# Optimization experiments

Hardware: AMD Instinct MI355X
Metric: run time of the kernel (lower is better)

The kernel has to match this reference:

```python
import jax, jax.numpy as jnp
import numpy as np

N, C, H, D, K = 16384, 256, 8, 64, 8
HID, OUT, NE = 512, 64, 64
COMMIT, RADIUS, RHID = 0.25, 10.0, 16


def setup_inputs() -> dict:
    key = jax.random.key(0)
    ks = jax.random.split(key, 20)
    def w(k, shape, fan_in):
        return jax.random.normal(k, shape, jnp.float32) / np.sqrt(fan_in).astype(np.float32)
    return {
        'x': jax.random.normal(ks[0], (N, C), jnp.float32),
        'coors': jax.random.normal(ks[1], (N, 3), jnp.float32) * 3.0,
        'nbr_idx': jax.random.randint(ks[2], (N, K), 0, N, jnp.int32),
        'Wq': w(ks[3], (C, H * D), C),
        'Wk': w(ks[4], (C, H * D), C),
        'Wv': w(ks[5], (C, H * D), C),
        'w_gate': w(ks[6], (C, H), C),
        'Wr1': w(ks[7], (1, RHID), 1),
        'br1': jnp.zeros((RHID,), jnp.float32),
        'Wr2': w(ks[8], (RHID, H), RHID),
        'br2': jnp.zeros((H,), jnp.float32),
        'Wo': w(ks[9], (H * D + H, C), H * D + H),
        'alpha1': jnp.float32(0.5) * jnp.ones((), jnp.float32),
        'gamma1': jnp.ones((C,), jnp.float32),
        'beta1': jnp.zeros((C,), jnp.float32),
        'Wlin': w(ks[10], (C, HID), C),
        'blin': jnp.zeros((HID,), jnp.float32),
        'alpha2': jnp.float32(0.5) * jnp.ones((), jnp.float32),
        'gamma2': jnp.ones((HID + 20,), jnp.float32),
        'beta2': jnp.zeros((HID + 20,), jnp.float32),
        'Wout': w(ks[11], (HID + 20, OUT), HID + 20),
        'bout': jnp.zeros((OUT,), jnp.float32),
        'codebook': jax.random.normal(ks[12], (NE, OUT), jnp.float32),
    }


def reference(x, coors, Wq, Wk, Wv, w_gate, Wr1, br1, Wr2, br2, Wo,
              alpha1, gamma1, beta1, Wlin, blin, alpha2, gamma2, beta2,
              Wout, bout, codebook, nbr_idx):
    # ---- SE(3)-equivariant sparse-neighbor attention (heads=8, dim_head=64, K=8) ----
    q = (x @ Wq).reshape(N, H, D)
    xn = x[nbr_idx]                                  # [N,K,C] neighbor gather
    k = (xn @ Wk).reshape(N, K, H, D)
    v = (xn @ Wv).reshape(N, K, H, D)
    rel = coors[nbr_idx] - coors[:, None, :]         # [N,K,3]
    dist = jnp.sqrt(jnp.sum(rel * rel, -1) + 1e-8)   # [N,K]
    unit = rel / dist[..., None]
    radial = jax.nn.gelu(dist[..., None] @ Wr1 + br1) @ Wr2 + br2   # [N,K,H]
    logits = jnp.einsum('nhd,nkhd->nkh', q, k) / np.float32(np.sqrt(D)) + radial
    logits = jnp.where((dist <= RADIUS)[..., None], logits, jnp.float32(-1e9))
    attn = jax.nn.softmax(logits, axis=1)            # over K neighbors
    out0 = jnp.einsum('nkh,nkhd->nhd', attn, v).reshape(N, H * D)   # degree-0
    gate = xn @ w_gate                               # [N,K,H]
    vec = jnp.einsum('nkh,nkx->nhx', attn * gate, unit)             # degree-1 [N,H,3]
    vecnorm = jnp.sqrt(jnp.sum(vec * vec, -1) + 1e-8)               # invariant [N,H]
    se3_out = x + jnp.concatenate([out0, vecnorm], -1) @ Wo         # residual
    # ---- lin: DynamicTanh -> Linear -> GELU ----
    h = jnp.tanh(alpha1 * se3_out) * gamma1 + beta1
    h = jax.nn.gelu(h @ Wlin + blin)
    # ---- out_dense: concat 20-dim aa feats, DynamicTanh -> Linear -> GELU -> Tanh ----
    h2 = jnp.concatenate([h, x[:, :20]], -1)
    h2 = jnp.tanh(alpha2 * h2) * gamma2 + beta2
    z = jnp.tanh(jax.nn.gelu(h2 @ Wout + bout))      # [N,OUT]
    # ---- VQ-EMA: nearest codebook entry, commitment loss, straight-through ----
    d2 = (jnp.sum(z * z, -1, keepdims=True)
          - 2.0 * z @ codebook.T
          + jnp.sum(codebook * codebook, -1))
    idx = jnp.argmin(d2, axis=-1)
    zq = codebook[idx]
    vq_loss = COMMIT * jnp.mean((z - jax.lax.stop_gradient(zq)) ** 2)
    z_quantized = z + jax.lax.stop_gradient(zq - z)
    return z_quantized, vq_loss
```

## Files before the change

### kernel.cpp

```cpp
#include <hip/hip_runtime.h>
#include <hip/hip_bf16.h>
#include <stdint.h>

#define NPTS 16384
#define CDIM 256
#define HEADS 8
#define KNBR 8
#define HIDD 512
#define OUTD 64
#define NEMB 64
#define RHIDD 16

typedef _Float16 half8 __attribute__((ext_vector_type(8)));
typedef float f32x4 __attribute__((ext_vector_type(4)));

__device__ __forceinline__ float gelu_tanh(float v) {
    float v3 = v * v * v;
    return 0.5f * v * (1.0f + tanhf(0.79788456080286535588f * (v + 0.044715f * v3)));
}

__device__ __forceinline__ void gload16(const void* g, void* l) {
    __builtin_amdgcn_global_load_lds((const __attribute__((address_space(1))) void*)g,
                                     (__attribute__((address_space(3))) void*)l, 16, 0, 0);
}

template <int EPI>
__launch_bounds__(256)
__global__ void gemm_split(const _Float16* __restrict__ A2, const _Float16* __restrict__ B2,
                           int Kpad, int KT,
                           void* __restrict__ Cout, int ldc,
                           const float* __restrict__ bias,
                           const float* __restrict__ res,
                           const float* __restrict__ alphap,
                           const float* __restrict__ gamma,
                           const float* __restrict__ beta,
                           const float* __restrict__ a2p,
                           const float* __restrict__ g2,
                           const float* __restrict__ b2,
                           void* __restrict__ aux) {
    __shared__ __align__(16) char lds[32768];

    const int tid = threadIdx.x;
    const int l = tid & 63, w = tid >> 6;
    const int g = l >> 4, r = l & 15;
    const int wr = w >> 1, wc = w & 1;
    const int m0 = blockIdx.y * 128;
    const int n0 = blockIdx.x * 128;
    const int ldA = 2 * Kpad;
    const int srow = l >> 3;
    const int sl = (l & 7) ^ srow;
    const int scol = (sl & 3) * 8 + ((sl >= 4) ? Kpad : 0);
    const int swz = (l & 7) << 4;
    const int aBase = (wr * 64 + r) * 128;
    const int bBase = 16384 + (wc * 64 + r) * 128;
    const int koh = (g << 4) ^ swz;
    const int kol = (64 | (g << 4)) ^ swz;

    f32x4 acc[4][4] = {};

    const _Float16* aS = A2 + (size_t)m0 * ldA + scol;
    const _Float16* bS = B2 + (size_t)n0 * ldA + scol;

    for (int t = 0; t < KT; ++t) {
        const int kk = t * 32;
        #pragma unroll
        for (int cc = 0; cc < 4; ++cc) {
            int ch = w * 4 + cc;
            int row = ch * 8 + srow;
            gload16(aS + (size_t)row * ldA + kk, lds + ch * 1024);
            gload16(bS + (size_t)row * ldA + kk, lds + 16384 + ch * 1024);
        }
        __syncthreads();
        half8 ah[4], bh[4], xf[4];
        #pragma unroll
        for (int i = 0; i < 4; ++i) ah[i] = *(const half8*)(lds + aBase + i * 2048 + koh);
        #pragma unroll
        for (int j = 0; j < 4; ++j) bh[j] = *(const half8*)(lds + bBase + j * 2048 + koh);
        #pragma unroll
        for (int i = 0; i < 4; ++i)
            #pragma unroll
            for (int j = 0; j < 4; ++j)
                acc[i][j] = __builtin_amdgcn_mfma_f32_16x16x32_f16(ah[i], bh[j], acc[i][j], 0, 0, 0);
        #pragma unroll
        for (int j = 0; j < 4; ++j) xf[j] = *(const half8*)(lds + bBase + j * 2048 + kol);
        #pragma unroll
        for (int i = 0; i < 4; ++i)
            #pragma unroll
            for (int j = 0; j < 4; ++j)
                acc[i][j] = __builtin_amdgcn_mfma_f32_16x16x32_f16(ah[i], xf[j], acc[i][j], 0, 0, 0);
        #pragma unroll
        for (int i = 0; i < 4; ++i) xf[i] = *(const half8*)(lds + aBase + i * 2048 + kol);
        #pragma unroll
        for (int i = 0; i < 4; ++i)
            #pragma unroll
            for (int j = 0; j < 4; ++j)
                acc[i][j] = __builtin_amdgcn_mfma_f32_16x16x32_f16(xf[i], bh[j], acc[i][j], 0, 0, 0);
        __syncthreads();
    }

    const float alp = (EPI == 1 || EPI == 2) ? alphap[0] : 0.f;
    #pragma unroll
    for (int i = 0; i < 4; ++i) {
        #pragma unroll
        for (int j = 0; j < 4; ++j) {
            const int gcol = n0 + wc * 64 + j * 16 + r;
            #pragma unroll
            for (int q = 0; q < 4; ++q) {
                const int row = m0 + wr * 64 + i * 16 + g * 4 + q;
                float v = acc[i][j][q];
                if (EPI == 0) {
                    if (gcol < 1536) {
                        ((float*)Cout)[(size_t)row * 1536 + gcol] = v;
                    } else if (gcol < 1544) {
                        ((float*)aux)[(size_t)row * 8 + (gcol - 1536)] = v;
                    }
                } else if (EPI == 1) {
                    v += res[(size_t)row * CDIM + gcol];
                    v = tanhf(alp * v) * gamma[gcol] + beta[gcol];
                    _Float16 hi = (_Float16)v;
                    _Float16 lo = (_Float16)(v - (float)hi);
                    _Float16* H = (_Float16*)Cout;
                    H[(size_t)row * 512 + gcol] = hi;
                    H[(size_t)row * 512 + 256 + gcol] = lo;
                    if (gcol < 64) {
                        int tc = 512 + gcol;
                        float tv = 0.f;
                        if (gcol < 20)
                            tv = tanhf(a2p[0] * res[(size_t)row * CDIM + gcol]) * g2[tc] + b2[tc];
                        _Float16 thi = (_Float16)tv;
                        _Float16 tlo = (_Float16)(tv - (float)thi);
                        _Float16* T = (_Float16*)aux;
                        T[(size_t)row * 1152 + tc] = thi;
                        T[(size_t)row * 1152 + 576 + tc] = tlo;
                    }
                } else if (EPI == 2) {
                    v = gelu_tanh(v + bias[gcol]);
                    v = tanhf(alp * v) * gamma[gcol] + beta[gcol];
                    _Float16 hi = (_Float16)v;
                    _Float16 lo = (_Float16)(v - (float)hi);
                    _Float16* H = (_Float16*)Cout;
                    H[(size_t)row * 1152 + gcol] = hi;
                    H[(size_t)row * 1152 + 576 + gcol] = lo;
                }
            }
        }
    }
}

__launch_bounds__(256)
__global__ void gemm_out_vq(const _Float16* __restrict__ A2, const _Float16* __restrict__ B2,
                            const float* __restrict__ bout, const float* __restrict__ cb,
                            float* __restrict__ outZ, float* __restrict__ partials) {
    __shared__ __align__(16) char lds[34816];
    __shared__ float psum[64];
    float* zL  = (float*)lds;
    float* cbL = (float*)(lds + 17408);

    const int tid = threadIdx.x;
    const int l = tid & 63, w = tid >> 6;
    const int g = l >> 4, r = l & 15;
    const int wr = w >> 1, wc = w & 1;
    const int m0 = blockIdx.x * 64;
    const int Kpad = 576;
    const int ldA = 1152;
    const int srow = l >> 3;
    const int sl = (l & 7) ^ srow;
    const int scol = (sl & 3) * 8 + ((sl >= 4) ? Kpad : 0);
    const int swz = (l & 7) << 4;
    const int aBase = (wr * 32 + r) * 128;
    const int bBase = 8192 + (wc * 32 + r) * 128;
    const int koh = (g << 4) ^ swz;
    const int kol = (64 | (g << 4)) ^ swz;

    f32x4 acc[2][2] = {};

    const _Float16* aS = A2 + (size_t)m0 * ldA + scol;
    const _Float16* bS = B2 + scol;

    for (int t = 0; t < 18; ++t) {
        const int kk = t * 32;
        #pragma unroll
        for (int cc = 0; cc < 2; ++cc) {
            int ch = w * 2 + cc;
            int row = ch * 8 + srow;
            gload16(aS + (size_t)row * ldA + kk, lds + ch * 1024);
            gload16(bS + (size_t)row * ldA + kk, lds + 8192 + ch * 1024);
        }
        __syncthreads();
        half8 ah[2], bh[2], xf[2];
        #pragma unroll
        for (int i = 0; i < 2; ++i) ah[i] = *(const half8*)(lds + aBase + i * 2048 + koh);
        #pragma unroll
        for (int j = 0; j < 2; ++j) bh[j] = *(const half8*)(lds + bBase + j * 2048 + koh);
        #pragma unroll
        for (int i = 0; i < 2; ++i)
            #pragma unroll
            for (int j = 0; j < 2; ++j)
                acc[i][j] = __builtin_amdgcn_mfma_f32_16x16x32_f16(ah[i], bh[j], acc[i][j], 0, 0, 0);
        #pragma unroll
        for (int j = 0; j < 2; ++j) xf[j] = *(const half8*)(lds + bBase + j * 2048 + kol);
        #pragma unroll
        for (int i = 0; i < 2; ++i)
            #pragma unroll
            for (int j = 0; j < 2; ++j)
                acc[i][j] = __builtin_amdgcn_mfma_f32_16x16x32_f16(ah[i], xf[j], acc[i][j], 0, 0, 0);
        #pragma unroll
        for (int i = 0; i < 2; ++i) xf[i] = *(const half8*)(lds + aBase + i * 2048 + kol);
        #pragma unroll
        for (int i = 0; i < 2; ++i)
            #pragma unroll
            for (int j = 0; j < 2; ++j)
                acc[i][j] = __builtin_amdgcn_mfma_f32_16x16x32_f16(xf[i], bh[j], acc[i][j], 0, 0, 0);
        __syncthreads();
    }

    #pragma unroll
    for (int i = 0; i < 2; ++i) {
        #pragma unroll
        for (int j = 0; j < 2; ++j) {
            int col = wc * 32 + j * 16 + r;
            #pragma unroll
            for (int q = 0; q < 4; ++q) {
                int rl = wr * 32 + i * 16 + g * 4 + q;
                zL[rl * 68 + col] = tanhf(gelu_tanh(acc[i][j][q] + bout[col]));
            }
        }
    }
    for (int i = tid; i < NEMB * OUTD / 4; i += 256) {
        float4 v = ((const float4*)cb)[i];
        int e = (i * 4) >> 6, c0 = (i * 4) & 63;
        cbL[e * 68 + c0 + 0] = v.x; cbL[e * 68 + c0 + 1] = v.y;
        cbL[e * 68 + c0 + 2] = v.z; cbL[e * 68 + c0 + 3] = v.w;
    }
    __syncthreads();
    if (tid < 64) {
        float cc = 0.f;
        #pragma unroll
        for (int d = 0; d < 64; ++d) { float cv = cbL[tid * 68 + d]; cc += cv * cv; }
        cbL[tid * 68 + 64] = cc;
    }
    __syncthreads();

    const int row = tid >> 2, part = tid & 3;
    float best = 1e30f;
    int bidx = 0;
    for (int e = part * 16; e < part * 16 + 16; ++e) {
        float dot = 0.f;
        #pragma unroll
        for (int d = 0; d < 64; ++d) dot += zL[row * 68 + d] * cbL[e * 68 + d];
        float sc = cbL[e * 68 + 64] - 2.f * dot;
        if (sc < best) { best = sc; bidx = e; }
    }
    #pragma unroll
    for (int m = 1; m <= 2; m <<= 1) {
        float ob = __shfl_xor(best, m, 64);
        int oi = __shfl_xor(bidx, m, 64);
        if (ob < best || (ob == best && oi < bidx)) { best = ob; bidx = oi; }
    }
    const int grow = m0 + row;
    float lsum = 0.f;
    #pragma unroll
    for (int u = 0; u < 16; ++u) {
        float cv = cbL[bidx * 68 + part * 16 + u];
        outZ[(size_t)grow * 64 + part * 16 + u] = cv;
        float df = zL[row * 68 + part * 16 + u] - cv;
        lsum += df * df;
    }
    lsum += __shfl_xor(lsum, 1, 64);
    lsum += __shfl_xor(lsum, 2, 64);
    if (part == 0) psum[row] = lsum;
    __syncthreads();
    if (tid < 64) {
        float v = psum[tid];
        #pragma unroll
        for (int m = 1; m < 64; m <<= 1) v += __shfl_xor(v, m, 64);
        if (tid == 0) partials[blockIdx.x] = v;
    }
}

__global__ void vq_reduce(const float* __restrict__ partials, float* __restrict__ out) {
    __shared__ float s[256];
    int tid = threadIdx.x;
    s[tid] = partials[tid];
    __syncthreads();
    for (int st = 128; st > 0; st >>= 1) {
        if (tid < st) s[tid] += s[tid + st];
        __syncthreads();
    }
    if (tid == 0) out[0] = 0.25f * s[0] / ((float)NPTS * (float)OUTD);
}

#define R0 (NPTS * CDIM)
#define S1 (1664 * 256)
#define S2 (256 * 576)
#define S3 (512 * 256)
#define S4 (64 * 576)
__global__ void prep(const float* __restrict__ x,
                     const float* __restrict__ Wq, const float* __restrict__ Wk,
                     const float* __restrict__ Wv, const float* __restrict__ w_gate,
                     const float* __restrict__ Wo, const float* __restrict__ Wlin,
                     const float* __restrict__ Wout,
                     _Float16* __restrict__ x2, _Float16* __restrict__ wqkv2,
                     _Float16* __restrict__ wo2, _Float16* __restrict__ wlin2,
                     _Float16* __restrict__ wout2) {
    for (int idx = blockIdx.x * 256 + threadIdx.x; idx < R0 + S1 + S2 + S3 + S4;
         idx += gridDim.x * 256) {
        float v; _Float16* dst; size_t o0, o1;
        if (idx < R0) {
            int n = idx >> 8, cc = idx & 255;
            v = x[idx];
            dst = x2; o0 = (size_t)n * 512 + cc; o1 = o0 + 256;
        } else if (idx < R0 + S1) {
            int t = idx - R0;
            int j = t >> 8, k = t & 255;
            if (j < 1536) {
                int jm = j & 511;
                const float* W = (j < 512) ? Wq : (j < 1024) ? Wk : Wv;
                v = W[(size_t)k * 512 + jm];
            } else if (j < 1544) {
                v = w_gate[(size_t)k * 8 + (j - 1536)];
            } else {
                v = 0.f;
            }
            dst = wqkv2; o0 = (size_t)j * 512 + k; o1 = o0 + 256;
        } else if (idx < R0 + S1 + S2) {
            int t = idx - R0 - S1;
            int j = t / 576, k = t - j * 576;
            v = (k < 520) ? Wo[(size_t)k * 256 + j] : 0.f;
            dst = wo2; o0 = (size_t)j * 1152 + k; o1 = o0 + 576;
        } else if (idx < R0 + S1 + S2 + S3) {
            int t = idx - R0 - S1 - S2;
            int j = t >> 8, k = t & 255;
            v = Wlin[(size_t)k * 512 + j];
            dst = wlin2; o0 = (size_t)j * 512 + k; o1 = o0 + 256;
        } else {
            int t = idx - R0 - S1 - S2 - S3;
            int j = t / 576, k = t - j * 576;
            v = (k < 532) ? Wout[(size_t)k * 64 + j] : 0.f;
            dst = wout2; o0 = (size_t)j * 1152 + k; o1 = o0 + 576;
        }
        _Float16 hi = (_Float16)v, lo = (_Float16)(v - (float)hi);
        dst[o0] = hi; dst[o1] = lo;
    }
}

__launch_bounds__(256)
__global__ void attn_kernel(const float* __restrict__ QKV, const float* __restrict__ G,
                            const float* __restrict__ coors, const int* __restrict__ nbr,
                            const float* __restrict__ Wr1, const float* __restrict__ br1,
                            const float* __restrict__ Wr2, const float* __restrict__ br2,
                            _Float16* __restrict__ att2) {
    __shared__ float unitL[4][8][3];
    __shared__ float distL[4][8];
    __shared__ float radH[4][8][16];

    const int tid = threadIdx.x;
    const int w = tid >> 6;
    const int lane = tid & 63;
    const int n = blockIdx.x * 4 + w;
    const int h = lane >> 3;
    const int c = lane & 7;

    int jreg[KNBR];
    #pragma unroll
    for (int k = 0; k < KNBR; ++k) jreg[k] = nbr[(size_t)n * KNBR + k];

    if (lane < KNBR) {
        int jj = jreg[lane];
        float rx = coors[(size_t)jj * 3 + 0] - coors[(size_t)n * 3 + 0];
        float ry = coors[(size_t)jj * 3 + 1] - coors[(size_t)n * 3 + 1];
        float rz = coors[(size_t)jj * 3 + 2] - coors[(size_t)n * 3 + 2];
        float d = sqrtf(rx * rx + ry * ry + rz * rz + 1e-8f);
        float inv = 1.0f / d;
        distL[w][lane] = d;
        unitL[w][lane][0] = rx * inv;
        unitL[w][lane][1] = ry * inv;
        unitL[w][lane][2] = rz * inv;
    }

    const float4* qp = (const float4*)(QKV + (size_t)n * 1536 + lane * 8);
    float4 q0 = qp[0], q1 = qp[1];
    float p[KNBR];
    #pragma unroll
    for (int k = 0; k < KNBR; ++k) {
        const float4* kp = (const float4*)(QKV + (size_t)jreg[k] * 1536 + 512 + lane * 8);
        float4 k0 = kp[0], k1 = kp[1];
        p[k] = q0.x * k0.x + q0.y * k0.y + q0.z * k0.z + q0.w * k0.w
             + q1.x * k1.x + q1.y * k1.y + q1.z * k1.z + q1.w * k1.w;
    }
    #pragma unroll
    for (int m = 1; m <= 4; m <<= 1) {
        #pragma unroll
        for (int k = 0; k < KNBR; ++k) p[k] += __shfl_xor(p[k], m, 64);
    }
    __syncthreads();

    #pragma unroll
    for (int rr = 0; rr < 2; ++rr) {
        int idx = lane + rr * 64;
        int k = idx >> 4, i = idx & 15;
        float hv = distL[w][k] * Wr1[i] + br1[i];
        radH[w][k][i] = gelu_tanh(hv);
    }
    __syncthreads();

    float lg[KNBR];
    float b2v = br2[h];
    #pragma unroll
    for (int k = 0; k < KNBR; ++k) {
        float rad = b2v;
        #pragma unroll
        for (int i = 0; i < RHIDD; ++i) rad += radH[w][k][i] * Wr2[i * HEADS + h];
        lg[k] = p[k] * 0.125f + rad;
        if (!(distL[w][k] <= 10.0f)) lg[k] = -1e9f;
    }
    float mx = lg[0];
    #pragma unroll
    for (int k = 1; k < KNBR; ++k) mx = fmaxf(mx, lg[k]);
    float a[KNBR];
    float s = 0.f;
    #pragma unroll
    for (int k = 0; k < KNBR; ++k) { a[k] = expf(lg[k] - mx); s += a[k]; }
    float is = 1.0f / s;
    #pragma unroll
    for (int k = 0; k < KNBR; ++k) a[k] *= is;

    float vx = 0.f, vy = 0.f, vz = 0.f;
    #pragma unroll
    for (int k = 0; k < KNBR; ++k) {
        float gg = G[(size_t)jreg[k] * HEADS + h];
        float ag = a[k] * gg;
        vx += ag * unitL[w][k][0];
        vy += ag * unitL[w][k][1];
        vz += ag * unitL[w][k][2];
    }
    float vn = sqrtf(vx * vx + vy * vy + vz * vz + 1e-8f);

    float4 o0 = {0.f, 0.f, 0.f, 0.f}, o1 = {0.f, 0.f, 0.f, 0.f};
    #pragma unroll
    for (int k = 0; k < KNBR; ++k) {
        const float4* vp = (const float4*)(QKV + (size_t)jreg[k] * 1536 + 1024 + lane * 8);
        float4 v0 = vp[0], v1 = vp[1];
        float ak = a[k];
        o0.x += ak * v0.x; o0.y += ak * v0.y; o0.z += ak * v0.z; o0.w += ak * v0.w;
        o1.x += ak * v1.x; o1.y += ak * v1.y; o1.z += ak * v1.z; o1.w += ak * v1.w;
    }

    float ov[8] = {o0.x, o0.y, o0.z, o0.w, o1.x, o1.y, o1.z, o1.w};
    half8 hi8, lo8;
    #pragma unroll
    for (int t = 0; t < 8; ++t) {
        _Float16 hi = (_Float16)ov[t];
        hi8[t] = hi;
        lo8[t] = (_Float16)(ov[t] - (float)hi);
    }
    *(half8*)(att2 + (size_t)n * 1152 + lane * 8) = hi8;
    *(half8*)(att2 + (size_t)n * 1152 + 576 + lane * 8) = lo8;
    if (c == 0) {
        _Float16 hi = (_Float16)vn, lo = (_Float16)(vn - (float)hi);
        att2[(size_t)n * 1152 + 512 + h] = hi;
        att2[(size_t)n * 1152 + 576 + 512 + h] = lo;
    }
    if (lane < 56) {
        att2[(size_t)n * 1152 + 520 + lane] = (_Float16)0.f;
        att2[(size_t)n * 1152 + 1096 + lane] = (_Float16)0.f;
    }
}

extern "C" void kernel_launch(void* const* d_in, const int* in_sizes, int n_in,
                              void* d_out, int out_size, void* d_ws, size_t ws_size,
                              hipStream_t stream) {
    const float* x      = (const float*)d_in[0];
    const float* coors  = (const float*)d_in[1];
    const int*   nbr    = (const int*)  d_in[2];
    const float* Wq     = (const float*)d_in[3];
    const float* Wk     = (const float*)d_in[4];
    const float* Wv     = (const float*)d_in[5];
    const float* w_gate = (const float*)d_in[6];
    const float* Wr1    = (const float*)d_in[7];
    const float* br1    = (const float*)d_in[8];
    const float* Wr2    = (const float*)d_in[9];
    const float* br2    = (const float*)d_in[10];
    const float* Wo     = (const float*)d_in[11];
    const float* alpha1 = (const float*)d_in[12];
    const float* gamma1 = (const float*)d_in[13];
    const float* beta1  = (const float*)d_in[14];
    const float* Wlin   = (const float*)d_in[15];
    const float* blin   = (const float*)d_in[16];
    const float* alpha2 = (const float*)d_in[17];
    const float* gamma2 = (const float*)d_in[18];
    const float* beta2  = (const float*)d_in[19];
    const float* Wout   = (const float*)d_in[20];
    const float* bout   = (const float*)d_in[21];
    const float* cb     = (const float*)d_in[22];

    char* wsb = (char*)d_ws;
    float*    QKV   = (float*)   (wsb + 0);
    _Float16* att2  = (_Float16*)(wsb + 100663296);
    _Float16* x2    = (_Float16*)(wsb + 138412032);
    _Float16* wqkv2 = (_Float16*)(wsb + 155189248);
    _Float16* wo2   = (_Float16*)(wsb + 156893184);
    _Float16* wlin2 = (_Float16*)(wsb + 157483008);
    _Float16* wout2 = (_Float16*)(wsb + 158007296);
    float*    G     = (float*)   (wsb + 158154752);
    float*    part  = (float*)   (wsb + 158679040);
    _Float16* h1s   = (_Float16*)(wsb + 0);
    _Float16* h2s   = (_Float16*)(wsb + 20299776);

    float* outZ    = (float*)d_out;
    float* outLoss = outZ + (size_t)NPTS * OUTD;

    dim3 blk(256);

    prep<<<dim3(2048), blk, 0, stream>>>(x, Wq, Wk, Wv, w_gate, Wo, Wlin, Wout,
                                         x2, wqkv2, wo2, wlin2, wout2);
    gemm_split<0><<<dim3(13, 128), blk, 0, stream>>>(x2, wqkv2, 256, 8, QKV, 1536,
        nullptr, nullptr, nullptr, nullptr, nullptr, nullptr, nullptr, nullptr, G);
    attn_kernel<<<dim3(NPTS / 4), blk, 0, stream>>>(QKV, G, coors, nbr, Wr1, br1, Wr2, br2, att2);
    gemm_split<1><<<dim3(2, 128), blk, 0, stream>>>(att2, wo2, 576, 18, h1s, 0,
        nullptr, x, alpha1, gamma1, beta1, alpha2, gamma2, beta2, h2s);
    gemm_split<2><<<dim3(4, 128), blk, 0, stream>>>(h1s, wlin2, 256, 8, h2s, 0,
        blin, nullptr, alpha2, gamma2, beta2, nullptr, nullptr, nullptr, nullptr);
    gemm_out_vq<<<dim3(256), blk, 0, stream>>>(h2s, wout2, bout, cb, outZ, part);
    vq_reduce<<<dim3(1), blk, 0, stream>>>(part, outLoss);
}
```

Measured before the change: 397.8 us.

## Double-buffer LDS tiles in later GEMMs and fold VQ loss reduction into atomics

```diff
diff --git a/kernel.cpp b/kernel.cpp
--- a/kernel.cpp
+++ b/kernel.cpp
@@ -24,7 +24,7 @@
                                      (__attribute__((address_space(3))) void*)l, 16, 0, 0);
 }
 
-template <int EPI>
+template <int EPI, int DBUF>
 __launch_bounds__(256)
 __global__ void gemm_split(const _Float16* __restrict__ A2, const _Float16* __restrict__ B2,
                            int Kpad, int KT,
@@ -38,7 +38,8 @@
                            const float* __restrict__ g2,
                            const float* __restrict__ b2,
                            void* __restrict__ aux) {
-    __shared__ __align__(16) char lds[32768];
+    constexpr int LBYTES = DBUF ? 65536 : 32768;
+    __shared__ __align__(16) char lds[LBYTES];
 
     const int tid = threadIdx.x;
     const int l = tid & 63, w = tid >> 6;
@@ -61,41 +62,66 @@
     const _Float16* aS = A2 + (size_t)m0 * ldA + scol;
     const _Float16* bS = B2 + (size_t)n0 * ldA + scol;
 
-    for (int t = 0; t < KT; ++t) {
+    auto stage = [&](int buf, int t) {
         const int kk = t * 32;
+        char* d0 = lds + buf * 32768;
         #pragma unroll
         for (int cc = 0; cc < 4; ++cc) {
             int ch = w * 4 + cc;
             int row = ch * 8 + srow;
-            gload16(aS + (size_t)row * ldA + kk, lds + ch * 1024);
-            gload16(bS + (size_t)row * ldA + kk, lds + 16384 + ch * 1024);
-        }
-        __syncthreads();
+            gload16(aS + (size_t)row * ldA + kk, d0 + ch * 1024);
+            gload16(bS + (size_t)row * ldA + kk, d0 + 16384 + ch * 1024);
+        }
+    };
+    auto passes = [&](const char* Lb) {
         half8 ah[4], bh[4], xf[4];
         #pragma unroll
-        for (int i = 0; i < 4; ++i) ah[i] = *(const half8*)(lds + aBase + i * 2048 + koh);
-        #pragma unroll
-        for (int j = 0; j < 4; ++j) bh[j] = *(const half8*)(lds + bBase + j * 2048 + koh);
+        for (int i = 0; i < 4; ++i) ah[i] = *(const half8*)(Lb + aBase + i * 2048 + koh);
+        #pragma unroll
+        for (int j = 0; j < 4; ++j) bh[j] = *(const half8*)(Lb + bBase + j * 2048 + koh);
         #pragma unroll
         for (int i = 0; i < 4; ++i)
             #pragma unroll
             for (int j = 0; j < 4; ++j)
                 acc[i][j] = __builtin_amdgcn_mfma_f32_16x16x32_f16(ah[i], bh[j], acc[i][j], 0, 0, 0);
         #pragma unroll
-        for (int j = 0; j < 4; ++j) xf[j] = *(const half8*)(lds + bBase + j * 2048 + kol);
+        for (int j = 0; j < 4; ++j) xf[j] = *(const half8*)(Lb + bBase + j * 2048 + kol);
         #pragma unroll
         for (int i = 0; i < 4; ++i)
             #pragma unroll
             for (int j = 0; j < 4; ++j)
                 acc[i][j] = __builtin_amdgcn_mfma_f32_16x16x32_f16(ah[i], xf[j], acc[i][j], 0, 0, 0);
         #pragma unroll
-        for (int i = 0; i < 4; ++i) xf[i] = *(const half8*)(lds + aBase + i * 2048 + kol);
+        for (int i = 0; i < 4; ++i) xf[i] = *(const half8*)(Lb + aBase + i * 2048 + kol);
         #pragma unroll
         for (int i = 0; i < 4; ++i)
             #pragma unroll
             for (int j = 0; j < 4; ++j)
                 acc[i][j] = __builtin_amdgcn_mfma_f32_16x16x32_f16(xf[i], bh[j], acc[i][j], 0, 0, 0);
-        __syncthreads();
+    };
+
+    if (DBUF) {
+        stage(0, 0);
+        for (int t = 0; t < KT; ++t) {
+            const int cur = t & 1;
+            if (t + 1 < KT) {
+                stage(cur ^ 1, t + 1);
+                asm volatile("s_waitcnt vmcnt(8)" ::: "memory");
+            } else {
+                asm volatile("s_waitcnt vmcnt(0)" ::: "memory");
+            }
+            __builtin_amdgcn_s_barrier();
+            __builtin_amdgcn_sched_barrier(0);
+            passes(lds + cur * 32768);
+            __builtin_amdgcn_s_barrier();
+        }
+    } else {
+        for (int t = 0; t < KT; ++t) {
+            stage(0, t);
+            __syncthreads();
+            passes(lds);
+            __syncthreads();
+        }
     }
 
     const float alp = (EPI == 1 || EPI == 2) ? alphap[0] : 0.f;
@@ -150,7 +176,7 @@
 __launch_bounds__(256)
 __global__ void gemm_out_vq(const _Float16* __restrict__ A2, const _Float16* __restrict__ B2,
                             const float* __restrict__ bout, const float* __restrict__ cb,
-                            float* __restrict__ outZ, float* __restrict__ partials) {
+                            float* __restrict__ outZ, float* __restrict__ outLoss) {
     __shared__ __align__(16) char lds[34816];
     __shared__ float psum[64];
     float* zL  = (float*)lds;
@@ -177,41 +203,55 @@
     const _Float16* aS = A2 + (size_t)m0 * ldA + scol;
     const _Float16* bS = B2 + scol;
 
-    for (int t = 0; t < 18; ++t) {
+    auto stage = [&](int buf, int t) {
         const int kk = t * 32;
+        char* d0 = lds + buf * 16384;
         #pragma unroll
         for (int cc = 0; cc < 2; ++cc) {
             int ch = w * 2 + cc;
             int row = ch * 8 + srow;
-            gload16(aS + (size_t)row * ldA + kk, lds + ch * 1024);
-            gload16(bS + (size_t)row * ldA + kk, lds + 8192 + ch * 1024);
-        }
-        __syncthreads();
+            gload16(aS + (size_t)row * ldA + kk, d0 + ch * 1024);
+            gload16(bS + (size_t)row * ldA + kk, d0 + 8192 + ch * 1024);
+        }
+    };
+
+    stage(0, 0);
+    for (int t = 0; t < 18; ++t) {
+        const int cur = t & 1;
+        if (t + 1 < 18) {
+            stage(cur ^ 1, t + 1);
+            asm volatile("s_waitcnt vmcnt(4)" ::: "memory");
+        } else {
+            asm volatile("s_waitcnt vmcnt(0)" ::: "memory");
+        }
+        __builtin_amdgcn_s_barrier();
+        __builtin_amdgcn_sched_barrier(0);
+        const char* Lb = lds + cur * 16384;
         half8 ah[2], bh[2], xf[2];
         #pragma unroll
-        for (int i = 0; i < 2; ++i) ah[i] = *(const half8*)(lds + aBase + i * 2048 + koh);
-        #pragma unroll
-        for (int j = 0; j < 2; ++j) bh[j] = *(const half8*)(lds + bBase + j * 2048 + koh);
+        for (int i = 0; i < 2; ++i) ah[i] = *(const half8*)(Lb + aBase + i * 2048 + koh);
+        #pragma unroll
+        for (int j = 0; j < 2; ++j) bh[j] = *(const half8*)(Lb + bBase + j * 2048 + koh);
         #pragma unroll
         for (int i = 0; i < 2; ++i)
             #pragma unroll
             for (int j = 0; j < 2; ++j)
                 acc[i][j] = __builtin_amdgcn_mfma_f32_16x16x32_f16(ah[i], bh[j], acc[i][j], 0, 0, 0);
         #pragma unroll
-        for (int j = 0; j < 2; ++j) xf[j] = *(const half8*)(lds + bBase + j * 2048 + kol);
+        for (int j = 0; j < 2; ++j) xf[j] = *(const half8*)(Lb + bBase + j * 2048 + kol);
         #pragma unroll
         for (int i = 0; i < 2; ++i)
             #pragma unroll
             for (int j = 0; j < 2; ++j)
                 acc[i][j] = __builtin_amdgcn_mfma_f32_16x16x32_f16(ah[i], xf[j], acc[i][j], 0, 0, 0);
         #pragma unroll
-        for (int i = 0; i < 2; ++i) xf[i] = *(const half8*)(lds + aBase + i * 2048 + kol);
+        for (int i = 0; i < 2; ++i) xf[i] = *(const half8*)(Lb + aBase + i * 2048 + kol);
         #pragma unroll
         for (int i = 0; i < 2; ++i)
             #pragma unroll
             for (int j = 0; j < 2; ++j)
                 acc[i][j] = __builtin_amdgcn_mfma_f32_16x16x32_f16(xf[i], bh[j], acc[i][j], 0, 0, 0);
-        __syncthreads();
+        __builtin_amdgcn_s_barrier();
     }
 
     #pragma unroll
@@ -274,20 +314,9 @@
         float v = psum[tid];
         #pragma unroll
         for (int m = 1; m < 64; m <<= 1) v += __shfl_xor(v, m, 64);
-        if (tid == 0) partials[blockIdx.x] = v;
-    }
-}
-
-__global__ void vq_reduce(const float* __restrict__ partials, float* __restrict__ out) {
-    __shared__ float s[256];
-    int tid = threadIdx.x;
-    s[tid] = partials[tid];
-    __syncthreads();
-    for (int st = 128; st > 0; st >>= 1) {
-        if (tid < st) s[tid] += s[tid + st];
-        __syncthreads();
-    }
-    if (tid == 0) out[0] = 0.25f * s[0] / ((float)NPTS * (float)OUTD);
+        if (tid == 0)
+            atomicAdd(outLoss, v * (0.25f / ((float)NPTS * (float)OUTD)));
+    }
 }
 
 #define R0 (NPTS * CDIM)
@@ -302,7 +331,8 @@
                      const float* __restrict__ Wout,
                      _Float16* __restrict__ x2, _Float16* __restrict__ wqkv2,
                      _Float16* __restrict__ wo2, _Float16* __restrict__ wlin2,
-                     _Float16* __restrict__ wout2) {
+                     _Float16* __restrict__ wout2, float* __restrict__ outLoss) {
+    if (blockIdx.x == 0 && threadIdx.x == 0) *outLoss = 0.f;
     for (int idx = blockIdx.x * 256 + threadIdx.x; idx < R0 + S1 + S2 + S3 + S4;
          idx += gridDim.x * 256) {
         float v; _Float16* dst; size_t o0, o1;
@@ -503,7 +533,6 @@
     _Float16* wlin2 = (_Float16*)(wsb + 157483008);
     _Float16* wout2 = (_Float16*)(wsb + 158007296);
     float*    G     = (float*)   (wsb + 158154752);
-    float*    part  = (float*)   (wsb + 158679040);
     _Float16* h1s   = (_Float16*)(wsb + 0);
     _Float16* h2s   = (_Float16*)(wsb + 20299776);
 
@@ -513,14 +542,13 @@
     dim3 blk(256);
 
     prep<<<dim3(2048), blk, 0, stream>>>(x, Wq, Wk, Wv, w_gate, Wo, Wlin, Wout,
-                                         x2, wqkv2, wo2, wlin2, wout2);
-    gemm_split<0><<<dim3(13, 128), blk, 0, stream>>>(x2, wqkv2, 256, 8, QKV, 1536,
+                                         x2, wqkv2, wo2, wlin2, wout2, outLoss);
+    gemm_split<0, 0><<<dim3(13, 128), blk, 0, stream>>>(x2, wqkv2, 256, 8, QKV, 1536,
         nullptr, nullptr, nullptr, nullptr, nullptr, nullptr, nullptr, nullptr, G);
     attn_kernel<<<dim3(NPTS / 4), blk, 0, stream>>>(QKV, G, coors, nbr, Wr1, br1, Wr2, br2, att2);
-    gemm_split<1><<<dim3(2, 128), blk, 0, stream>>>(att2, wo2, 576, 18, h1s, 0,
+    gemm_split<1, 1><<<dim3(2, 128), blk, 0, stream>>>(att2, wo2, 576, 18, h1s, 0,
         nullptr, x, alpha1, gamma1, beta1, alpha2, gamma2, beta2, h2s);
-    gemm_split<2><<<dim3(4, 128), blk, 0, stream>>>(h1s, wlin2, 256, 8, h2s, 0,
+    gemm_split<2, 1><<<dim3(4, 128), blk, 0, stream>>>(h1s, wlin2, 256, 8, h2s, 0,
         blin, nullptr, alpha2, gamma2, beta2, nullptr, nullptr, nullptr, nullptr);
-    gemm_out_vq<<<dim3(256), blk, 0, stream>>>(h2s, wout2, bout, cb, outZ, part);
-    vq_reduce<<<dim3(1), blk, 0, stream>>>(part, outLoss);
-}
+    gemm_out_vq<<<dim3(256), blk, 0, stream>>>(h2s, wout2, bout, cb, outZ, outLoss);
+}
```

Measured after the change: 379.9 us. -4.5%, faster.

## Fuse Wo, Wlin, Wout GEMMs and VQ into one per-row-tile tail kernel

Applied to the files above, without the earlier changes.

```diff
diff --git a/kernel.cpp b/kernel.cpp
--- a/kernel.cpp
+++ b/kernel.cpp
@@ -24,20 +24,9 @@
                                      (__attribute__((address_space(3))) void*)l, 16, 0, 0);
 }
 
-template <int EPI>
 __launch_bounds__(256)
-__global__ void gemm_split(const _Float16* __restrict__ A2, const _Float16* __restrict__ B2,
-                           int Kpad, int KT,
-                           void* __restrict__ Cout, int ldc,
-                           const float* __restrict__ bias,
-                           const float* __restrict__ res,
-                           const float* __restrict__ alphap,
-                           const float* __restrict__ gamma,
-                           const float* __restrict__ beta,
-                           const float* __restrict__ a2p,
-                           const float* __restrict__ g2,
-                           const float* __restrict__ b2,
-                           void* __restrict__ aux) {
+__global__ void gemm_qkv(const _Float16* __restrict__ A2, const _Float16* __restrict__ B2,
+                         float* __restrict__ QKV, float* __restrict__ G) {
     __shared__ __align__(16) char lds[32768];
 
     const int tid = threadIdx.x;
@@ -46,10 +35,10 @@
     const int wr = w >> 1, wc = w & 1;
     const int m0 = blockIdx.y * 128;
     const int n0 = blockIdx.x * 128;
-    const int ldA = 2 * Kpad;
+    const int ldA = 512;
     const int srow = l >> 3;
     const int sl = (l & 7) ^ srow;
-    const int scol = (sl & 3) * 8 + ((sl >= 4) ? Kpad : 0);
+    const int scol = (sl & 3) * 8 + ((sl >= 4) ? 256 : 0);
     const int swz = (l & 7) << 4;
     const int aBase = (wr * 64 + r) * 128;
     const int bBase = 16384 + (wc * 64 + r) * 128;
@@ -61,7 +50,7 @@
     const _Float16* aS = A2 + (size_t)m0 * ldA + scol;
     const _Float16* bS = B2 + (size_t)n0 * ldA + scol;
 
-    for (int t = 0; t < KT; ++t) {
+    for (int t = 0; t < 8; ++t) {
         const int kk = t * 32;
         #pragma unroll
         for (int cc = 0; cc < 4; ++cc) {
@@ -98,7 +87,6 @@
         __syncthreads();
     }
 
-    const float alp = (EPI == 1 || EPI == 2) ? alphap[0] : 0.f;
     #pragma unroll
     for (int i = 0; i < 4; ++i) {
         #pragma unroll
@@ -108,39 +96,10 @@
             for (int q = 0; q < 4; ++q) {
                 const int row = m0 + wr * 64 + i * 16 + g * 4 + q;
                 float v = acc[i][j][q];
-                if (EPI == 0) {
-                    if (gcol < 1536) {
-                        ((float*)Cout)[(size_t)row * 1536 + gcol] = v;
-                    } else if (gcol < 1544) {
-                        ((float*)aux)[(size_t)row * 8 + (gcol - 1536)] = v;
-                    }
-                } else if (EPI == 1) {
-                    v += res[(size_t)row * CDIM + gcol];
-                    v = tanhf(alp * v) * gamma[gcol] + beta[gcol];
-                    _Float16 hi = (_Float16)v;
-                    _Float16 lo = (_Float16)(v - (float)hi);
-                    _Float16* H = (_Float16*)Cout;
-                    H[(size_t)row * 512 + gcol] = hi;
-                    H[(size_t)row * 512 + 256 + gcol] = lo;
-                    if (gcol < 64) {
-                        int tc = 512 + gcol;
-                        float tv = 0.f;
-                        if (gcol < 20)
-                            tv = tanhf(a2p[0] * res[(size_t)row * CDIM + gcol]) * g2[tc] + b2[tc];
-                        _Float16 thi = (_Float16)tv;
-                        _Float16 tlo = (_Float16)(tv - (float)thi);
-                        _Float16* T = (_Float16*)aux;
-                        T[(size_t)row * 1152 + tc] = thi;
-                        T[(size_t)row * 1152 + 576 + tc] = tlo;
-                    }
-                } else if (EPI == 2) {
-                    v = gelu_tanh(v + bias[gcol]);
-                    v = tanhf(alp * v) * gamma[gcol] + beta[gcol];
-                    _Float16 hi = (_Float16)v;
-                    _Float16 lo = (_Float16)(v - (float)hi);
-                    _Float16* H = (_Float16*)Cout;
-                    H[(size_t)row * 1152 + gcol] = hi;
-                    H[(size_t)row * 1152 + 576 + gcol] = lo;
+                if (gcol < 1536) {
+                    QKV[(size_t)row * 1536 + gcol] = v;
+                } else if (gcol < 1544) {
+                    G[(size_t)row * 8 + (gcol - 1536)] = v;
                 }
             }
         }
@@ -148,82 +107,233 @@
 }
 
 __launch_bounds__(256)
-__global__ void gemm_out_vq(const _Float16* __restrict__ A2, const _Float16* __restrict__ B2,
-                            const float* __restrict__ bout, const float* __restrict__ cb,
-                            float* __restrict__ outZ, float* __restrict__ partials) {
-    __shared__ __align__(16) char lds[34816];
-    __shared__ float psum[64];
-    float* zL  = (float*)lds;
-    float* cbL = (float*)(lds + 17408);
+__global__ void mega_tail(const _Float16* __restrict__ att2,
+                          const _Float16* __restrict__ wo2,
+                          const _Float16* __restrict__ wlin2,
+                          const _Float16* __restrict__ wout2,
+                          const float* __restrict__ x,
+                          const float* __restrict__ alpha1p, const float* __restrict__ gamma1,
+                          const float* __restrict__ beta1, const float* __restrict__ blin,
+                          const float* __restrict__ alpha2p, const float* __restrict__ gamma2,
+                          const float* __restrict__ beta2, const float* __restrict__ bout,
+                          const float* __restrict__ cb,
+                          float* __restrict__ outZ, float* __restrict__ outLoss) {
+    __shared__ __align__(16) char lds[122880];
+    char* const h1L = lds;
+    char* const R1  = lds + 32768;
+    char* const R2  = lds + 106496;
 
     const int tid = threadIdx.x;
     const int l = tid & 63, w = tid >> 6;
     const int g = l >> 4, r = l & 15;
     const int wr = w >> 1, wc = w & 1;
-    const int m0 = blockIdx.x * 64;
-    const int Kpad = 576;
-    const int ldA = 1152;
+    const int m0 = blockIdx.x * 32;
     const int srow = l >> 3;
     const int sl = (l & 7) ^ srow;
-    const int scol = (sl & 3) * 8 + ((sl >= 4) ? Kpad : 0);
-    const int swz = (l & 7) << 4;
-    const int aBase = (wr * 32 + r) * 128;
-    const int bBase = 8192 + (wc * 32 + r) * 128;
+    const int scol576 = (sl & 3) * 8 + ((sl >= 4) ? 576 : 0);
+    const int scol256 = (sl & 3) * 8 + ((sl >= 4) ? 256 : 0);
+    const int swz = (r & 7) << 4;
     const int koh = (g << 4) ^ swz;
     const int kol = (64 | (g << 4)) ^ swz;
-
-    f32x4 acc[2][2] = {};
-
-    const _Float16* aS = A2 + (size_t)m0 * ldA + scol;
-    const _Float16* bS = B2 + scol;
-
-    for (int t = 0; t < 18; ++t) {
-        const int kk = t * 32;
-        #pragma unroll
-        for (int cc = 0; cc < 2; ++cc) {
-            int ch = w * 2 + cc;
-            int row = ch * 8 + srow;
-            gload16(aS + (size_t)row * ldA + kk, lds + ch * 1024);
-            gload16(bS + (size_t)row * ldA + kk, lds + 8192 + ch * 1024);
-        }
-        __syncthreads();
-        half8 ah[2], bh[2], xf[2];
-        #pragma unroll
-        for (int i = 0; i < 2; ++i) ah[i] = *(const half8*)(lds + aBase + i * 2048 + koh);
-        #pragma unroll
-        for (int j = 0; j < 2; ++j) bh[j] = *(const half8*)(lds + bBase + j * 2048 + koh);
-        #pragma unroll
-        for (int i = 0; i < 2; ++i)
-            #pragma unroll
-            for (int j = 0; j < 2; ++j)
-                acc[i][j] = __builtin_amdgcn_mfma_f32_16x16x32_f16(ah[i], bh[j], acc[i][j], 0, 0, 0);
-        #pragma unroll
-        for (int j = 0; j < 2; ++j) xf[j] = *(const half8*)(lds + bBase + j * 2048 + kol);
-        #pragma unroll
-        for (int i = 0; i < 2; ++i)
-            #pragma unroll
-            for (int j = 0; j < 2; ++j)
-                acc[i][j] = __builtin_amdgcn_mfma_f32_16x16x32_f16(ah[i], xf[j], acc[i][j], 0, 0, 0);
-        #pragma unroll
-        for (int i = 0; i < 2; ++i) xf[i] = *(const half8*)(lds + aBase + i * 2048 + kol);
-        #pragma unroll
-        for (int i = 0; i < 2; ++i)
-            #pragma unroll
-            for (int j = 0; j < 2; ++j)
-                acc[i][j] = __builtin_amdgcn_mfma_f32_16x16x32_f16(xf[i], bh[j], acc[i][j], 0, 0, 0);
-        __syncthreads();
-    }
-
-    #pragma unroll
-    for (int i = 0; i < 2; ++i) {
-        #pragma unroll
-        for (int j = 0; j < 2; ++j) {
-            int col = wc * 32 + j * 16 + r;
-            #pragma unroll
-            for (int q = 0; q < 4; ++q) {
-                int rl = wr * 32 + i * 16 + g * 4 + q;
-                zL[rl * 68 + col] = tanhf(gelu_tanh(acc[i][j][q] + bout[col]));
-            }
+    const float a1 = alpha1p[0], a2 = alpha2p[0];
+
+    f32x4 acc0[8] = {};
+    {
+        auto stage0 = [&](int buf, int kt) {
+            char* d = R1 + buf * 36864;
+            const int kk = kt * 32;
+            gload16(att2 + (size_t)(m0 + w * 8 + srow) * 1152 + kk + scol576, d + w * 1024);
+            #pragma unroll
+            for (int i = 0; i < 8; ++i) {
+                int ch = w * 8 + i;
+                gload16(wo2 + (size_t)(ch * 8 + srow) * 1152 + kk + scol576,
+                        d + 4096 + ch * 1024);
+            }
+        };
+        stage0(0, 0);
+        for (int kt = 0; kt < 18; ++kt) {
+            const int cur = kt & 1;
+            if (kt + 1 < 18) {
+                stage0(cur ^ 1, kt + 1);
+                asm volatile("s_waitcnt vmcnt(9)" ::: "memory");
+            } else {
+                asm volatile("s_waitcnt vmcnt(0)" ::: "memory");
+            }
+            __builtin_amdgcn_s_barrier();
+            __builtin_amdgcn_sched_barrier(0);
+            const char* d = R1 + cur * 36864;
+            const int arow = wr * 16 + r;
+            const char* aAddr = d + (arow >> 3) * 1024 + (arow & 7) * 128;
+            half8 a_h = *(const half8*)(aAddr + koh);
+            half8 a_l = *(const half8*)(aAddr + kol);
+            #pragma unroll
+            for (int jf = 0; jf < 8; ++jf) {
+                const int brow = wc * 128 + jf * 16 + r;
+                const char* bAddr = d + 4096 + (brow >> 3) * 1024 + (brow & 7) * 128;
+                half8 b_h = *(const half8*)(bAddr + koh);
+                half8 b_l = *(const half8*)(bAddr + kol);
+                acc0[jf] = __builtin_amdgcn_mfma_f32_16x16x32_f16(a_h, b_h, acc0[jf], 0, 0, 0);
+                acc0[jf] = __builtin_amdgcn_mfma_f32_16x16x32_f16(a_h, b_l, acc0[jf], 0, 0, 0);
+                acc0[jf] = __builtin_amdgcn_mfma_f32_16x16x32_f16(a_l, b_h, acc0[jf], 0, 0, 0);
+            }
+            __builtin_amdgcn_s_barrier();
+        }
+    }
+    #pragma unroll
+    for (int jf = 0; jf < 8; ++jf) {
+        #pragma unroll
+        for (int q = 0; q < 4; ++q) {
+            const int row = wr * 16 + g * 4 + q;
+            const int col = wc * 128 + jf * 16 + r;
+            float v = acc0[jf][q] + x[(size_t)(m0 + row) * CDIM + col];
+            v = tanhf(a1 * v) * gamma1[col] + beta1[col];
+            _Float16 hi = (_Float16)v;
+            _Float16 lo = (_Float16)(v - (float)hi);
+            const int ktw = col >> 5, kloc = col & 31;
+            const int Lhi = ((kloc >> 3) << 4) | ((kloc & 7) << 1);
+            const int sw = (row & 7) << 4;
+            char* base = h1L + ktw * 4096 + (row >> 3) * 1024 + (row & 7) * 128;
+            *(_Float16*)(base + (Lhi ^ sw)) = hi;
+            *(_Float16*)(base + ((Lhi | 64) ^ sw)) = lo;
+        }
+    }
+    {
+        const int rw = tid >> 3, c8 = tid & 7;
+        #pragma unroll
+        for (int u = 0; u < 8; ++u) {
+            const int col = c8 * 8 + u;
+            float v = 0.f;
+            if (col < 20)
+                v = tanhf(a2 * x[(size_t)(m0 + rw) * CDIM + col]) * gamma2[512 + col] + beta2[512 + col];
+            _Float16 hi = (_Float16)v;
+            _Float16 lo = (_Float16)(v - (float)hi);
+            const int ktw = 16 + (col >> 5), kloc = col & 31;
+            const int Lhi = ((kloc >> 3) << 4) | ((kloc & 7) << 1);
+            const int sw = (rw & 7) << 4;
+            char* base = R1 + ktw * 4096 + (rw >> 3) * 1024 + (rw & 7) * 128;
+            *(_Float16*)(base + (Lhi ^ sw)) = hi;
+            *(_Float16*)(base + ((Lhi | 64) ^ sw)) = lo;
+        }
+    }
+    __syncthreads();
+
+    {
+        f32x4 accB[2] = {};
+        accB[0] = (f32x4){0.f, 0.f, 0.f, 0.f};
+        accB[1] = (f32x4){0.f, 0.f, 0.f, 0.f};
+        auto stageB = [&](int it) {
+            const int c2 = it >> 3, kt2 = it & 7;
+            char* d = R2 + (it & 1) * 8192;
+            #pragma unroll
+            for (int i = 0; i < 2; ++i) {
+                int ch = w * 2 + i;
+                gload16(wlin2 + (size_t)(c2 * 64 + ch * 8 + srow) * 512 + kt2 * 32 + scol256,
+                        d + ch * 1024);
+            }
+        };
+        stageB(0);
+        for (int it = 0; it < 64; ++it) {
+            if (it + 1 < 64) {
+                stageB(it + 1);
+                asm volatile("s_waitcnt vmcnt(2)" ::: "memory");
+            } else {
+                asm volatile("s_waitcnt vmcnt(0)" ::: "memory");
+            }
+            __builtin_amdgcn_s_barrier();
+            __builtin_amdgcn_sched_barrier(0);
+            const int kt = it & 7;
+            const char* d = R2 + (it & 1) * 8192;
+            const int arow = wr * 16 + r;
+            const char* aAddr = h1L + kt * 4096 + (arow >> 3) * 1024 + (arow & 7) * 128;
+            half8 a_h = *(const half8*)(aAddr + koh);
+            half8 a_l = *(const half8*)(aAddr + kol);
+            #pragma unroll
+            for (int jf = 0; jf < 2; ++jf) {
+                const int brow = wc * 32 + jf * 16 + r;
+                const char* bAddr = d + (brow >> 3) * 1024 + (brow & 7) * 128;
+                half8 b_h = *(const half8*)(bAddr + koh);
+                half8 b_l = *(const half8*)(bAddr + kol);
+                accB[jf] = __builtin_amdgcn_mfma_f32_16x16x32_f16(a_h, b_h, accB[jf], 0, 0, 0);
+                accB[jf] = __builtin_amdgcn_mfma_f32_16x16x32_f16(a_h, b_l, accB[jf], 0, 0, 0);
+                accB[jf] = __builtin_amdgcn_mfma_f32_16x16x32_f16(a_l, b_h, accB[jf], 0, 0, 0);
+            }
+            if ((it & 7) == 7) {
+                const int c2 = it >> 3;
+                #pragma unroll
+                for (int jf = 0; jf < 2; ++jf) {
+                    #pragma unroll
+                    for (int q = 0; q < 4; ++q) {
+                        const int row = wr * 16 + g * 4 + q;
+                        const int colg = c2 * 64 + wc * 32 + jf * 16 + r;
+                        float v = gelu_tanh(accB[jf][q] + blin[colg]);
+                        v = tanhf(a2 * v) * gamma2[colg] + beta2[colg];
+                        _Float16 hi = (_Float16)v;
+                        _Float16 lo = (_Float16)(v - (float)hi);
+                        const int ktw = colg >> 5, kloc = colg & 31;
+                        const int Lhi = ((kloc >> 3) << 4) | ((kloc & 7) << 1);
+                        const int sw = (row & 7) << 4;
+                        char* base = R1 + ktw * 4096 + (row >> 3) * 1024 + (row & 7) * 128;
+                        *(_Float16*)(base + (Lhi ^ sw)) = hi;
+                        *(_Float16*)(base + ((Lhi | 64) ^ sw)) = lo;
+                    }
+                    accB[jf] = (f32x4){0.f, 0.f, 0.f, 0.f};
+                }
+            }
+            __builtin_amdgcn_s_barrier();
+        }
+    }
+    __syncthreads();
+
+    f32x4 accC[2] = {};
+    {
+        auto stageC = [&](int kt) {
+            char* d = R2 + (kt & 1) * 8192;
+            #pragma unroll
+            for (int i = 0; i < 2; ++i) {
+                int ch = w * 2 + i;
+                gload16(wout2 + (size_t)(ch * 8 + srow) * 1152 + kt * 32 + scol576,
+                        d + ch * 1024);
+            }
+        };
+        stageC(0);
+        for (int kt = 0; kt < 18; ++kt) {
+            if (kt + 1 < 18) {
+                stageC(kt + 1);
+                asm volatile("s_waitcnt vmcnt(2)" ::: "memory");
+            } else {
+                asm volatile("s_waitcnt vmcnt(0)" ::: "memory");
+            }
+            __builtin_amdgcn_s_barrier();
+            __builtin_amdgcn_sched_barrier(0);
+            const char* d = R2 + (kt & 1) * 8192;
+            const int arow = wr * 16 + r;
+            const char* aAddr = R1 + kt * 4096 + (arow >> 3) * 1024 + (arow & 7) * 128;
+            half8 a_h = *(const half8*)(aAddr + koh);
+            half8 a_l = *(const half8*)(aAddr + kol);
+            #pragma unroll
+            for (int jf = 0; jf < 2; ++jf) {
+                const int brow = wc * 32 + jf * 16 + r;
+                const char* bAddr = d + (brow >> 3) * 1024 + (brow & 7) * 128;
+                half8 b_h = *(const half8*)(bAddr + koh);
+                half8 b_l = *(const half8*)(bAddr + kol);
+                accC[jf] = __builtin_amdgcn_mfma_f32_16x16x32_f16(a_h, b_h, accC[jf], 0, 0, 0);
+                accC[jf] = __builtin_amdgcn_mfma_f32_16x16x32_f16(a_h, b_l, accC[jf], 0, 0, 0);
+                accC[jf] = __builtin_amdgcn_mfma_f32_16x16x32_f16(a_l, b_h, accC[jf], 0, 0, 0);
+            }
+            __builtin_amdgcn_s_barrier();
+        }
+    }
+
+    float* zL   = (float*)lds;
+    float* cbL  = (float*)(lds + 8704);
+    float* psum = (float*)(lds + 26112);
+    #pragma unroll
+    for (int jf = 0; jf < 2; ++jf) {
+        #pragma unroll
+        for (int q = 0; q < 4; ++q) {
+            const int row = wr * 16 + g * 4 + q;
+            const int col = wc * 32 + jf * 16 + r;
+            zL[row * 68 + col] = tanhf(gelu_tanh(accC[jf][q] + bout[col]));
         }
     }
     for (int i = tid; i < NEMB * OUTD / 4; i += 256) {
@@ -241,10 +351,10 @@
     }
     __syncthreads();
 
-    const int row = tid >> 2, part = tid & 3;
+    const int row = tid >> 3, part = tid & 7;
     float best = 1e30f;
     int bidx = 0;
-    for (int e = part * 16; e < part * 16 + 16; ++e) {
+    for (int e = part * 8; e < part * 8 + 8; ++e) {
         float dot = 0.f;
         #pragma unroll
         for (int d = 0; d < 64; ++d) dot += zL[row * 68 + d] * cbL[e * 68 + d];
@@ -252,45 +362,35 @@
         if (sc < best) { best = sc; bidx = e; }
     }
     #pragma unroll
-    for (int m = 1; m <= 2; m <<= 1) {
+    for (int m = 1; m <= 4; m <<= 1) {
         float ob = __shfl_xor(best, m, 64);
         int oi = __shfl_xor(bidx, m, 64);
         if (ob < best || (ob == best && oi < bidx)) { best = ob; bidx = oi; }
     }
-    const int grow = m0 + row;
     float lsum = 0.f;
     #pragma unroll
-    for (int u = 0; u < 16; ++u) {
-        float cv = cbL[bidx * 68 + part * 16 + u];
-        outZ[(size_t)grow * 64 + part * 16 + u] = cv;
-        float df = zL[row * 68 + part * 16 + u] - cv;
+    for (int u = 0; u < 8; ++u) {
+        const int col = part * 8 + u;
+        float cv = cbL[bidx * 68 + col];
+        outZ[(size_t)(m0 + row) * 64 + col] = cv;
+        float df = zL[row * 68 + col] - cv;
         lsum += df * df;
     }
     lsum += __shfl_xor(lsum, 1, 64);
     lsum += __shfl_xor(lsum, 2, 64);
+    lsum += __shfl_xor(lsum, 4, 64);
     if (part == 0) psum[row] = lsum;
     __syncthreads();
-    if (tid < 64) {
+    if (tid < 32) {
         float v = psum[tid];
         #pragma unroll
-        for (int m = 1; m < 64; m <<= 1) v += __shfl_xor(v, m, 64);
-        if (tid == 0) partials[blockIdx.x] = v;
+        for (int m = 1; m < 32; m <<= 1) v += __shfl_xor(v, m, 64);
+        if (tid == 0)
+            atomicAdd(outLoss, v * (0.25f / ((float)NPTS * (float)OUTD)));
     }
 }
 
-__global__ void vq_reduce(const float* __restrict__ partials, float* __restrict__ out) {
-    __shared__ float s[256];
-    int tid = threadIdx.x;
-    s[tid] = partials[tid];
-    __syncthreads();
-    for (int st = 128; st > 0; st >>= 1) {
-        if (tid < st) s[tid] += s[tid + st];
-        __syncthreads();
-    }
-    if (tid == 0) out[0] = 0.25f * s[0] / ((float)NPTS * (float)OUTD);
-}
-
-#define R0 (NPTS * CDIM)
+#define R0SZ (NPTS * CDIM)
 #define S1 (1664 * 256)
 #define S2 (256 * 576)
 #define S3 (512 * 256)
@@ -302,16 +402,17 @@
                      const float* __restrict__ Wout,
                      _Float16* __restrict__ x2, _Float16* __restrict__ wqkv2,
                      _Float16* __restrict__ wo2, _Float16* __restrict__ wlin2,
-                     _Float16* __restrict__ wout2) {
-    for (int idx = blockIdx.x * 256 + threadIdx.x; idx < R0 + S1 + S2 + S3 + S4;
+                     _Float16* __restrict__ wout2, float* __restrict__ outLoss) {
+    if (blockIdx.x == 0 && threadIdx.x == 0) *outLoss = 0.f;
+    for (int idx = blockIdx.x * 256 + threadIdx.x; idx < R0SZ + S1 + S2 + S3 + S4;
          idx += gridDim.x * 256) {
         float v; _Float16* dst; size_t o0, o1;
-        if (idx < R0) {
+        if (idx < R0SZ) {
             int n = idx >> 8, cc = idx & 255;
             v = x[idx];
             dst = x2; o0 = (size_t)n * 512 + cc; o1 = o0 + 256;
-        } else if (idx < R0 + S1) {
-            int t = idx - R0;
+        } else if (idx < R0SZ + S1) {
+            int t = idx - R0SZ;
             int j = t >> 8, k = t & 255;
             if (j < 1536) {
                 int jm = j & 511;
@@ -323,18 +424,18 @@
                 v = 0.f;
             }
             dst = wqkv2; o0 = (size_t)j * 512 + k; o1 = o0 + 256;
-        } else if (idx < R0 + S1 + S2) {
-            int t = idx - R0 - S1;
+        } else if (idx < R0SZ + S1 + S2) {
+            int t = idx - R0SZ - S1;
             int j = t / 576, k = t - j * 576;
             v = (k < 520) ? Wo[(size_t)k * 256 + j] : 0.f;
             dst = wo2; o0 = (size_t)j * 1152 + k; o1 = o0 + 576;
-        } else if (idx < R0 + S1 + S2 + S3) {
-            int t = idx - R0 - S1 - S2;
+        } else if (idx < R0SZ + S1 + S2 + S3) {
+            int t = idx - R0SZ - S1 - S2;
             int j = t >> 8, k = t & 255;
             v = Wlin[(size_t)k * 512 + j];
             dst = wlin2; o0 = (size_t)j * 512 + k; o1 = o0 + 256;
         } else {
-            int t = idx - R0 - S1 - S2 - S3;
+            int t = idx - R0SZ - S1 - S2 - S3;
             int j = t / 576, k = t - j * 576;
             v = (k < 532) ? Wout[(size_t)k * 64 + j] : 0.f;
             dst = wout2; o0 = (size_t)j * 1152 + k; o1 = o0 + 576;
@@ -503,9 +604,6 @@
     _Float16* wlin2 = (_Float16*)(wsb + 157483008);
     _Float16* wout2 = (_Float16*)(wsb + 158007296);
     float*    G     = (float*)   (wsb + 158154752);
-    float*    part  = (float*)   (wsb + 158679040);
-    _Float16* h1s   = (_Float16*)(wsb + 0);
-    _Float16* h2s   = (_Float16*)(wsb + 20299776);
 
     float* outZ    = (float*)d_out;
     float* outLoss = outZ + (size_t)NPTS * OUTD;
@@ -513,14 +611,9 @@
     dim3 blk(256);
 
     prep<<<dim3(2048), blk, 0, stream>>>(x, Wq, Wk, Wv, w_gate, Wo, Wlin, Wout,
-                                         x2, wqkv2, wo2, wlin2, wout2);
-    gemm_split<0><<<dim3(13, 128), blk, 0, stream>>>(x2, wqkv2, 256, 8, QKV, 1536,
-        nullptr, nullptr, nullptr, nullptr, nullptr, nullptr, nullptr, nullptr, G);
+                                         x2, wqkv2, wo2, wlin2, wout2, outLoss);
+    gemm_qkv<<<dim3(13, 128), blk, 0, stream>>>(x2, wqkv2, QKV, G);
     attn_kernel<<<dim3(NPTS / 4), blk, 0, stream>>>(QKV, G, coors, nbr, Wr1, br1, Wr2, br2, att2);
-    gemm_split<1><<<dim3(2, 128), blk, 0, stream>>>(att2, wo2, 576, 18, h1s, 0,
-        nullptr, x, alpha1, gamma1, beta1, alpha2, gamma2, beta2, h2s);
-    gemm_split<2><<<dim3(4, 128), blk, 0, stream>>>(h1s, wlin2, 256, 8, h2s, 0,
-        blin, nullptr, alpha2, gamma2, beta2, nullptr, nullptr, nullptr, nullptr);
-    gemm_out_vq<<<dim3(256), blk, 0, stream>>>(h2s, wout2, bout, cb, outZ, part);
-    vq_reduce<<<dim3(1), blk, 0, stream>>>(part, outLoss);
+    mega_tail<<<dim3(NPTS / 32), blk, 0, stream>>>(att2, wo2, wlin2, wout2, x,
+        alpha1, gamma1, beta1, blin, alpha2, gamma2, beta2, bout, cb, outZ, outLoss);
 }
```

Result: no change. 400.8 us (+0.8%).
